# Kernel tuning notes

Hardware: AMD Instinct MI355X
Metric: run time of the kernel (lower is better)

## Reference

```python
import jax, jax.numpy as jnp
import numpy as np

B, D, H, Q, N, V = 2048, 2048, 16, 128, 8192, 128


def setup_inputs() -> dict:
    key = jax.random.key(0)
    k1, k2, k3, k4, k5 = jax.random.split(key, 5)
    return {
        "x": jax.random.normal(k1, (B, D), dtype=jnp.float32),
        "keys": jax.random.normal(k2, (N, Q), dtype=jnp.float32),
        "values": jax.random.normal(k3, (N, V), dtype=jnp.float32),
        "Wq": jax.random.normal(k4, (H * Q, D), dtype=jnp.float32) * (1.0 / np.sqrt(D)),
        "Wo": jax.random.normal(k5, (D, H * V), dtype=jnp.float32) * (1.0 / np.sqrt(H * V)),
    }


def reference(x, keys, values, Wq, Wo):
    b = x.shape[0]
    h, q = H, Q
    # queries: [B, H, Q]
    queries = (x @ Wq.T).reshape(b, h, q)
    # einsum 'aib,ajb->aijb' then sum over last axis == dot product over Q
    scores = jnp.einsum('bhq,nq->bhn', queries, keys) / jnp.sqrt(jnp.asarray(q, x.dtype))
    attn = jax.nn.softmax(scores, axis=-1)  # [B, H, N]
    # Original: einsum('aib,ajc->aijc', attn, values) sums attn over its N axis
    # (label b) independently of values' N axis (label j), giving
    # out[a,i,j,c] = attn_rowsum[a,i] * values[j,c]; mean over j then yields
    # attn_rowsum[a,i] * mean_n(values)[c]. Computed here without the [B,H,N,V]
    # intermediate (mathematically identical).
    attn_rowsum = attn.sum(axis=-1)        # [B, H] (== 1 up to fp error)
    vmean = values.mean(axis=0)            # [V]
    outv = (attn_rowsum[:, :, None] * vmean[None, None, :]).reshape(b, -1)  # [B, H*V]
    return outv @ Wo.T + x
```

## Files before the change

kernel.cpp:

```cpp
#include <hip/hip_runtime.h>


#define NROWS 8192
#define VDIM  128
#define DDIM  2048
#define BDIM  2048
#define P_ROWS 128

__global__ void prep_kernel(const float4* __restrict__ vals4,
                            const float4* __restrict__ Wo4,
                            float4* __restrict__ partial4,
                            float4* __restrict__ WoF4) {
    __shared__ float4 s[256];
    const int t = threadIdx.x;
    const int b = blockIdx.x;

    if (b < P_ROWS) {
        float4 acc = make_float4(0.f, 0.f, 0.f, 0.f);
        const int base = b * 2048;
#pragma unroll
        for (int j = 0; j < 8; ++j) {
            float4 v = vals4[base + t + 256 * j];
            acc.x += v.x; acc.y += v.y; acc.z += v.z; acc.w += v.w;
        }
        s[t] = acc;
        __syncthreads();
        if (t < 32) {
            float4 r = s[t];
#pragma unroll
            for (int k = 1; k < 8; ++k) {
                float4 v = s[t + 32 * k];
                r.x += v.x; r.y += v.y; r.z += v.z; r.w += v.w;
            }
            partial4[b * 32 + t] = r;
        }
    } else {
        const int wb = b - P_ROWS;
        const int vq = t & 31;
        const int hg = t >> 5;
        for (int d = wb; d < DDIM; d += 896) {
            const float4* row = Wo4 + (size_t)d * 512;
            float4 a = row[(2 * hg) * 32 + vq];
            float4 c = row[(2 * hg + 1) * 32 + vq];
            a.x += c.x; a.y += c.y; a.z += c.z; a.w += c.w;
            s[t] = a;
            __syncthreads();
            if (t < 32) {
                float4 r = s[t];
#pragma unroll
                for (int k = 1; k < 8; ++k) {
                    float4 v = s[t + 32 * k];
                    r.x += v.x; r.y += v.y; r.z += v.z; r.w += v.w;
                }
                WoF4[d * 32 + t] = r;
            }
            __syncthreads();
        }
    }
}

__global__ void c_add_kernel(const float4* __restrict__ partial4,
                             const float4* __restrict__ WoF4,
                             const float4* __restrict__ x4,
                             float4* __restrict__ out4) {
    __shared__ float4 s[256];
    __shared__ float4 vm_lds[32];
    __shared__ float  c_lds[128];
    const int t = threadIdx.x;
    const int dc = blockIdx.x & 15;
    const int rg = blockIdx.x >> 4;

    float4 acc = make_float4(0.f, 0.f, 0.f, 0.f);
#pragma unroll
    for (int j = 0; j < 16; ++j) {
        float4 v = partial4[t + 256 * j];
        acc.x += v.x; acc.y += v.y; acc.z += v.z; acc.w += v.w;
    }
    s[t] = acc;
    __syncthreads();
    if (t < 32) {
        float4 r = s[t];
#pragma unroll
        for (int k = 1; k < 8; ++k) {
            float4 v = s[t + 32 * k];
            r.x += v.x; r.y += v.y; r.z += v.z; r.w += v.w;
        }
        const float inv = 1.0f / (float)NROWS;
        r.x *= inv; r.y *= inv; r.z *= inv; r.w *= inv;
        vm_lds[t] = r;
    }
    __syncthreads();

    {
        const int ld = t >> 1;
        const int half = t & 1;
        const size_t base = (size_t)(dc * 128 + ld) * 32 + half * 16;
        float dot = 0.f;
#pragma unroll
        for (int j = 0; j < 16; ++j) {
            float4 w = WoF4[base + j];
            float4 vm = vm_lds[half * 16 + j];
            dot += w.x * vm.x + w.y * vm.y + w.z * vm.z + w.w * vm.w;
        }
        dot += __shfl_xor(dot, 1);
        if (half == 0) c_lds[ld] = dot;
    }
    __syncthreads();

    const float4* __restrict__ c4 = (const float4*)c_lds;
    const int q = t & 31;
    const int r0 = rg * 32 + (t >> 5);
    const float4 cv = c4[q];
#pragma unroll
    for (int i = 0; i < 4; ++i) {
        const int r = r0 + i * 8;
        const size_t idx = (size_t)r * 512 + dc * 32 + q;
        float4 xv = x4[idx];
        xv.x += cv.x; xv.y += cv.y; xv.z += cv.z; xv.w += cv.w;
        out4[idx] = xv;
    }
}

extern "C" void kernel_launch(void* const* d_in, const int* in_sizes, int n_in,
                              void* d_out, int out_size, void* d_ws, size_t ws_size,
                              hipStream_t stream) {
    const float* x      = (const float*)d_in[0];
    const float* values = (const float*)d_in[2];
    const float* Wo     = (const float*)d_in[4];
    float* out = (float*)d_out;
    float* ws  = (float*)d_ws;

    float4* partial4 = (float4*)ws;
    float4* WoF4     = (float4*)(ws + P_ROWS * VDIM);

    prep_kernel<<<1024, 256, 0, stream>>>((const float4*)values, (const float4*)Wo,
                                          partial4, WoF4);
    c_add_kernel<<<1024, 256, 0, stream>>>(partial4, WoF4,
                                           (const float4*)x, (float4*)out);
}
```

Baseline: 24.59 us.

## Split c-vector computation from broadcast add into separate kernels

Before, each of the 1024 add blocks redundantly reduced all value partials and recomputed a 128-wide slice of the c vector. Now a small 32-block kernel computes the full c vector once into workspace, and a separate 2048-block kernel streams x and adds c. The prep kernel is also rebalanced to 256 value blocks and 768 Wo blocks. This removes the repeated reduction work but adds a third kernel launch and an extra serial dependency.

```diff
diff --git a/kernel.cpp b/kernel.cpp
--- a/kernel.cpp
+++ b/kernel.cpp
@@ -5,21 +5,24 @@
 #define VDIM  128
 #define DDIM  2048
 #define BDIM  2048
-#define P_ROWS 128
+#define VBLK  256
+#define WBLK  768
 
-__global__ void prep_kernel(const float4* __restrict__ vals4,
-                            const float4* __restrict__ Wo4,
-                            float4* __restrict__ partial4,
-                            float4* __restrict__ WoF4) {
+__global__ void __launch_bounds__(256) prep_kernel(
+    const float4* __restrict__ vals4,
+    const float4* __restrict__ Wo4,
+    float4* __restrict__ partial4,
+    float4* __restrict__ WoF4)
+{
     __shared__ float4 s[256];
     const int t = threadIdx.x;
-    const int b = blockIdx.x;
+    const int bid = blockIdx.x;
 
-    if (b < P_ROWS) {
+    if (bid < VBLK) {
         float4 acc = make_float4(0.f, 0.f, 0.f, 0.f);
-        const int base = b * 2048;
+        const int base = bid * 1024;
 #pragma unroll
-        for (int j = 0; j < 8; ++j) {
+        for (int j = 0; j < 4; ++j) {
             float4 v = vals4[base + t + 256 * j];
             acc.x += v.x; acc.y += v.y; acc.z += v.z; acc.w += v.w;
         }
@@ -32,17 +35,17 @@
                 float4 v = s[t + 32 * k];
                 r.x += v.x; r.y += v.y; r.z += v.z; r.w += v.w;
             }
-            partial4[b * 32 + t] = r;
+            partial4[bid * 32 + t] = r;
         }
     } else {
-        const int wb = b - P_ROWS;
+        const int wb = bid - VBLK;
         const int vq = t & 31;
         const int hg = t >> 5;
-        for (int d = wb; d < DDIM; d += 896) {
+        for (int d = wb; d < DDIM; d += WBLK) {
             const float4* row = Wo4 + (size_t)d * 512;
             float4 a = row[(2 * hg) * 32 + vq];
-            float4 c = row[(2 * hg + 1) * 32 + vq];
-            a.x += c.x; a.y += c.y; a.z += c.z; a.w += c.w;
+            float4 b = row[(2 * hg + 1) * 32 + vq];
+            a.x += b.x; a.y += b.y; a.z += b.z; a.w += b.w;
             s[t] = a;
             __syncthreads();
             if (t < 32) {
@@ -59,20 +62,18 @@
     }
 }
 
-__global__ void c_add_kernel(const float4* __restrict__ partial4,
-                             const float4* __restrict__ WoF4,
-                             const float4* __restrict__ x4,
-                             float4* __restrict__ out4) {
+__global__ void __launch_bounds__(256) c_kernel(
+    const float4* __restrict__ partial4,
+    const float4* __restrict__ WoF4,
+    float* __restrict__ cvec)
+{
     __shared__ float4 s[256];
     __shared__ float4 vm_lds[32];
-    __shared__ float  c_lds[128];
     const int t = threadIdx.x;
-    const int dc = blockIdx.x & 15;
-    const int rg = blockIdx.x >> 4;
 
     float4 acc = make_float4(0.f, 0.f, 0.f, 0.f);
 #pragma unroll
-    for (int j = 0; j < 16; ++j) {
+    for (int j = 0; j < 32; ++j) {
         float4 v = partial4[t + 256 * j];
         acc.x += v.x; acc.y += v.y; acc.z += v.z; acc.w += v.w;
     }
@@ -91,34 +92,37 @@
     }
     __syncthreads();
 
-    {
-        const int ld = t >> 1;
-        const int half = t & 1;
-        const size_t base = (size_t)(dc * 128 + ld) * 32 + half * 16;
-        float dot = 0.f;
+    const int dl = t >> 2;
+    const int part = t & 3;
+    const int d = blockIdx.x * 64 + dl;
+    float dot = 0.f;
 #pragma unroll
-        for (int j = 0; j < 16; ++j) {
-            float4 w = WoF4[base + j];
-            float4 vm = vm_lds[half * 16 + j];
-            dot += w.x * vm.x + w.y * vm.y + w.z * vm.z + w.w * vm.w;
-        }
-        dot += __shfl_xor(dot, 1);
-        if (half == 0) c_lds[ld] = dot;
+    for (int j = 0; j < 8; ++j) {
+        float4 w = WoF4[(size_t)d * 32 + part * 8 + j];
+        float4 vm = vm_lds[part * 8 + j];
+        dot += w.x * vm.x + w.y * vm.y + w.z * vm.z + w.w * vm.w;
     }
-    __syncthreads();
+    dot += __shfl_xor(dot, 1);
+    dot += __shfl_xor(dot, 2);
+    if (part == 0) cvec[d] = dot;
+}
 
-    const float4* __restrict__ c4 = (const float4*)c_lds;
-    const int q = t & 31;
-    const int r0 = rg * 32 + (t >> 5);
-    const float4 cv = c4[q];
-#pragma unroll
-    for (int i = 0; i < 4; ++i) {
-        const int r = r0 + i * 8;
-        const size_t idx = (size_t)r * 512 + dc * 32 + q;
-        float4 xv = x4[idx];
-        xv.x += cv.x; xv.y += cv.y; xv.z += cv.z; xv.w += cv.w;
-        out4[idx] = xv;
-    }
+__global__ void __launch_bounds__(256) add_kernel(
+    const float4* __restrict__ x4,
+    const float* __restrict__ cvec,
+    float4* __restrict__ out4)
+{
+    const float4* __restrict__ c4 = (const float4*)cvec;
+    const int t = threadIdx.x;
+    const size_t base = (size_t)blockIdx.x * 512 + t;
+    float4 xv0 = x4[base];
+    float4 xv1 = x4[base + 256];
+    float4 cv0 = c4[t];
+    float4 cv1 = c4[t + 256];
+    xv0.x += cv0.x; xv0.y += cv0.y; xv0.z += cv0.z; xv0.w += cv0.w;
+    xv1.x += cv1.x; xv1.y += cv1.y; xv1.z += cv1.z; xv1.w += cv1.w;
+    out4[base] = xv0;
+    out4[base + 256] = xv1;
 }
 
 extern "C" void kernel_launch(void* const* d_in, const int* in_sizes, int n_in,
@@ -131,10 +135,12 @@
     float* ws  = (float*)d_ws;
 
     float4* partial4 = (float4*)ws;
-    float4* WoF4     = (float4*)(ws + P_ROWS * VDIM);
+    float4* WoF4     = (float4*)(ws + 32768);
+    float*  cvec     = ws + 32768 + 262144;
 
-    prep_kernel<<<1024, 256, 0, stream>>>((const float4*)values, (const float4*)Wo,
-                                          partial4, WoF4);
-    c_add_kernel<<<1024, 256, 0, stream>>>(partial4, WoF4,
-                                           (const float4*)x, (float4*)out);
+    prep_kernel<<<VBLK + WBLK, 256, 0, stream>>>((const float4*)values,
+                                                 (const float4*)Wo,
+                                                 partial4, WoF4);
+    c_kernel<<<32, 256, 0, stream>>>(partial4, WoF4, cvec);
+    add_kernel<<<2048, 256, 0, stream>>>((const float4*)x, cvec, (float4*)out);
 }
```

After: 20.56 us. -16.4%, faster.
